# Performance work log

Hardware: AMD Instinct MI355X
Metric: run time of the kernel (lower is better)

## Reference

```python
import jax, jax.numpy as jnp
import numpy as np

N_ATOMS = 500_000
N_DOMAINS = 250_000
N_ENTRIES = 4_000_000
C_IN = 64
C_OUT = 128


def setup_inputs() -> dict:
    key = jax.random.key(0)
    k1, k2, k3, k4 = jax.random.split(key, 4)
    features = jax.random.normal(k1, (N_ATOMS, C_IN), dtype=jnp.float32)
    atom_indices = jax.random.randint(k2, (N_ENTRIES,), 0, N_ATOMS, dtype=jnp.int64)
    domain_ids = jnp.sort(jax.random.randint(k3, (N_ENTRIES,), 0, N_DOMAINS, dtype=jnp.int64))
    # Linear params: xavier_uniform for w, zeros for b (per Linear.reset_parameters)
    limit = jnp.sqrt(6.0 / (C_IN + C_OUT)).astype(jnp.float32)
    W = jax.random.uniform(k4, (C_IN, C_OUT), dtype=jnp.float32, minval=-limit, maxval=limit)
    b = jnp.zeros((C_OUT,), dtype=jnp.float32)
    return {
        "features": features,
        "atom_indices": atom_indices,
        "domain_ids": domain_ids,
        "num_domains": N_DOMAINS,
        "W": W,
        "b": b,
    }


def reference(features, atom_indices, domain_ids, num_domains, W, b):
    # transfer0 (sum reduction): each target domain sums the ptensor0 features
    # of the source atoms it contains. Irregular gather + segment-reduce.
    gathered = features[atom_indices]                       # [E, C_in]
    transferred = jax.ops.segment_sum(gathered, domain_ids,
                                      num_segments=num_domains)  # [M, C_in]
    # Linear projection (mult_factor(0,0)=1 so in_channels unchanged)
    return transferred @ W + b                              # [M, C_out]
```

## Files before the change

kernel.cpp:

```cpp
#include <hip/hip_runtime.h>

__global__ void bounds_kernel(const int* __restrict__ dids,
                              int* __restrict__ starts,
                              int* __restrict__ ends, int E) {
    int e = blockIdx.x * blockDim.x + threadIdx.x;
    if (e >= E) return;
    int d = dids[e];
    if (e == 0) {
        starts[d] = 0;
    } else {
        int dp = dids[e - 1];
        if (d != dp) {
            starts[d] = e;
            ends[dp]  = e;
        }
    }
    if (e == E - 1) ends[d] = E;
}

__global__ void seg_sum_kernel(const float* __restrict__ feat,
                               const int* __restrict__ aidx,
                               const int* __restrict__ starts,
                               const int* __restrict__ ends,
                               float* __restrict__ T, int M) {
    int wid  = (int)(((size_t)blockIdx.x * blockDim.x + threadIdx.x) >> 6);
    if (wid >= M) return;
    int lane = threadIdx.x & 63;
    int g    = lane >> 4;
    int l16  = lane & 15;
    int coff = l16 * 4;

    int s = starts[wid];
    int e = ends[wid];

    float4 acc = make_float4(0.f, 0.f, 0.f, 0.f);
    if (s >= 0) {
        int last = e - 1;
        for (int base = s; base < e; base += 16) {
            int rem = e - base;
            int ti  = base + l16;
            int idxv = aidx[ti <= last ? ti : last];
            if (rem >= 16) {
#pragma unroll
                for (int p = 0; p < 4; ++p) {
                    int row = __shfl(idxv, p * 4 + g, 64);
                    const float4 v =
                        *(const float4*)(feat + (size_t)row * 64 + coff);
                    acc.x += v.x; acc.y += v.y; acc.z += v.z; acc.w += v.w;
                }
            } else {
                int nph = (rem + 3) >> 2;
                for (int p = 0; p < nph; ++p) {
                    int t   = base + p * 4 + g;
                    int row = __shfl(idxv, p * 4 + g, 64);
                    const float4 v =
                        *(const float4*)(feat + (size_t)row * 64 + coff);
                    float w = (t <= last) ? 1.f : 0.f;
                    acc.x = fmaf(v.x, w, acc.x);
                    acc.y = fmaf(v.y, w, acc.y);
                    acc.z = fmaf(v.z, w, acc.z);
                    acc.w = fmaf(v.w, w, acc.w);
                }
            }
        }
        acc.x += __shfl_xor(acc.x, 16, 64);
        acc.y += __shfl_xor(acc.y, 16, 64);
        acc.z += __shfl_xor(acc.z, 16, 64);
        acc.w += __shfl_xor(acc.w, 16, 64);
        acc.x += __shfl_xor(acc.x, 32, 64);
        acc.y += __shfl_xor(acc.y, 32, 64);
        acc.z += __shfl_xor(acc.z, 32, 64);
        acc.w += __shfl_xor(acc.w, 32, 64);
    }
    if (g == 0)
        *(float4*)(T + (size_t)wid * 64 + coff) = acc;
}

#define TM 128
__global__ void __launch_bounds__(256)
proj_kernel(const float* __restrict__ T,
            const float* __restrict__ W,
            const float* __restrict__ bias,
            float* __restrict__ out, int M) {
    __shared__ float lds_w[64][128];
    __shared__ float lds_t[64][TM + 4];

    int tid  = threadIdx.x;
    long row0 = (long)blockIdx.x * TM;

#pragma unroll
    for (int i = 0; i < 8; ++i) {
        int idx = tid + i * 256;
        int k   = idx >> 5;
        int ch  = idx & 31;
        float4 wv = ((const float4*)W)[idx];
        *(float4*)&lds_w[k][ch * 4] = wv;
    }
#pragma unroll
    for (int i = 0; i < 8; ++i) {
        int idx = tid + i * 256;
        int r   = idx >> 4;
        int ch  = idx & 15;
        long gr = row0 + r;
        if (gr > (long)M - 1) gr = (long)M - 1;
        float4 tv = ((const float4*)(T + gr * 64))[ch];
        lds_t[ch * 4 + 0][r] = tv.x;
        lds_t[ch * 4 + 1][r] = tv.y;
        lds_t[ch * 4 + 2][r] = tv.z;
        lds_t[ch * 4 + 3][r] = tv.w;
    }
    __syncthreads();

    int c0 = (tid & 15) * 8;
    int r0 = (tid >> 4) * 8;

    float acc[8][8];
#pragma unroll
    for (int r = 0; r < 8; ++r)
#pragma unroll
        for (int c = 0; c < 8; ++c) acc[r][c] = 0.f;

#pragma unroll 4
    for (int k = 0; k < 64; ++k) {
        float4 ta = *(const float4*)&lds_t[k][r0];
        float4 tb = *(const float4*)&lds_t[k][r0 + 4];
        float4 wa = *(const float4*)&lds_w[k][c0];
        float4 wb = *(const float4*)&lds_w[k][c0 + 4];
        float t[8] = {ta.x, ta.y, ta.z, ta.w, tb.x, tb.y, tb.z, tb.w};
        float w[8] = {wa.x, wa.y, wa.z, wa.w, wb.x, wb.y, wb.z, wb.w};
#pragma unroll
        for (int r = 0; r < 8; ++r)
#pragma unroll
            for (int c = 0; c < 8; ++c)
                acc[r][c] = fmaf(t[r], w[c], acc[r][c]);
    }

    float4 bva = *(const float4*)&bias[c0];
    float4 bvb = *(const float4*)&bias[c0 + 4];
#pragma unroll
    for (int r = 0; r < 8; ++r) {
        long row = row0 + r0 + r;
        if (row < M) {
            float4 o0, o1;
            o0.x = acc[r][0] + bva.x;
            o0.y = acc[r][1] + bva.y;
            o0.z = acc[r][2] + bva.z;
            o0.w = acc[r][3] + bva.w;
            o1.x = acc[r][4] + bvb.x;
            o1.y = acc[r][5] + bvb.y;
            o1.z = acc[r][6] + bvb.z;
            o1.w = acc[r][7] + bvb.w;
            *(float4*)&out[row * 128 + c0]     = o0;
            *(float4*)&out[row * 128 + c0 + 4] = o1;
        }
    }
}

extern "C" void kernel_launch(void* const* d_in, const int* in_sizes, int n_in,
                              void* d_out, int out_size, void* d_ws, size_t ws_size,
                              hipStream_t stream) {
    const float* feat = (const float*)d_in[0];
    const int*   aidx = (const int*)d_in[1];
    const int*   dids = (const int*)d_in[2];
    const float* W    = (const float*)d_in[4];
    const float* bias = (const float*)d_in[5];
    float*       out  = (float*)d_out;

    int E = in_sizes[1];
    int M = out_size / 128;

    float* T = (float*)d_ws;
    size_t tbytes = (size_t)M * 64 * sizeof(float);
    size_t bbytes = 2 * (size_t)M * sizeof(int);

    int* starts;
    if (ws_size >= tbytes + bbytes) {
        starts = (int*)((char*)d_ws + tbytes);
    } else {
        starts = (int*)((char*)d_out + (size_t)out_size * sizeof(float) - bbytes);
    }
    int* ends = starts + M;

    hipMemsetAsync(starts, 0xFF, bbytes, stream);

    bounds_kernel<<<(E + 255) / 256, 256, 0, stream>>>(dids, starts, ends, E);

    int waves_blocks = (int)(((size_t)M * 64 + 255) / 256);
    seg_sum_kernel<<<waves_blocks, 256, 0, stream>>>(feat, aidx, starts, ends, T, M);

    proj_kernel<<<(M + TM - 1) / TM, 256, 0, stream>>>(T, W, bias, out, M);
}
```

Measured before the change: 420.0 us.

## Fuse segment-sum gather with linear projection into a single kernel

Replaces the separate segment-sum and projection kernels with one fused kernel. Each 256-thread block gathers and reduces 128 domains into shared memory, four waves each handling 32 domains in sequence, then runs the 64x128 GEMM tile straight from shared memory. The projection loop is also reorganized to read row-major tiles in float4 chunks of k. This removes the global write and re-read of the intermediate M×64 tensor, but the large shared-memory footprint limits waves per CU during the latency-bound random gather.

After: 580.8 us. +38.3%, slower.

```diff
diff --git a/kernel.cpp b/kernel.cpp
--- a/kernel.cpp
+++ b/kernel.cpp
@@ -18,75 +18,39 @@
     if (e == E - 1) ends[d] = E;
 }
 
-__global__ void seg_sum_kernel(const float* __restrict__ feat,
-                               const int* __restrict__ aidx,
-                               const int* __restrict__ starts,
-                               const int* __restrict__ ends,
-                               float* __restrict__ T, int M) {
-    int wid  = (int)(((size_t)blockIdx.x * blockDim.x + threadIdx.x) >> 6);
-    if (wid >= M) return;
-    int lane = threadIdx.x & 63;
-    int g    = lane >> 4;
-    int l16  = lane & 15;
-    int coff = l16 * 4;
+#define DPB 128
 
-    int s = starts[wid];
-    int e = ends[wid];
+#define KSTEP(J, COMP)                                               \
+    {                                                                \
+        float4 wa = *(const float4*)&lds_w[kq * 4 + J][c0];          \
+        float4 wb = *(const float4*)&lds_w[kq * 4 + J][c0 + 4];      \
+        _Pragma("unroll")                                            \
+        for (int r = 0; r < 8; ++r) {                                \
+            float tv = tr[r].COMP;                                   \
+            acc[r][0] = fmaf(tv, wa.x, acc[r][0]);                   \
+            acc[r][1] = fmaf(tv, wa.y, acc[r][1]);                   \
+            acc[r][2] = fmaf(tv, wa.z, acc[r][2]);                   \
+            acc[r][3] = fmaf(tv, wa.w, acc[r][3]);                   \
+            acc[r][4] = fmaf(tv, wb.x, acc[r][4]);                   \
+            acc[r][5] = fmaf(tv, wb.y, acc[r][5]);                   \
+            acc[r][6] = fmaf(tv, wb.z, acc[r][6]);                   \
+            acc[r][7] = fmaf(tv, wb.w, acc[r][7]);                   \
+        }                                                            \
+    }
 
-    float4 acc = make_float4(0.f, 0.f, 0.f, 0.f);
-    if (s >= 0) {
-        int last = e - 1;
-        for (int base = s; base < e; base += 16) {
-            int rem = e - base;
-            int ti  = base + l16;
-            int idxv = aidx[ti <= last ? ti : last];
-            if (rem >= 16) {
-#pragma unroll
-                for (int p = 0; p < 4; ++p) {
-                    int row = __shfl(idxv, p * 4 + g, 64);
-                    const float4 v =
-                        *(const float4*)(feat + (size_t)row * 64 + coff);
-                    acc.x += v.x; acc.y += v.y; acc.z += v.z; acc.w += v.w;
-                }
-            } else {
-                int nph = (rem + 3) >> 2;
-                for (int p = 0; p < nph; ++p) {
-                    int t   = base + p * 4 + g;
-                    int row = __shfl(idxv, p * 4 + g, 64);
-                    const float4 v =
-                        *(const float4*)(feat + (size_t)row * 64 + coff);
-                    float w = (t <= last) ? 1.f : 0.f;
-                    acc.x = fmaf(v.x, w, acc.x);
-                    acc.y = fmaf(v.y, w, acc.y);
-                    acc.z = fmaf(v.z, w, acc.z);
-                    acc.w = fmaf(v.w, w, acc.w);
-                }
-            }
-        }
-        acc.x += __shfl_xor(acc.x, 16, 64);
-        acc.y += __shfl_xor(acc.y, 16, 64);
-        acc.z += __shfl_xor(acc.z, 16, 64);
-        acc.w += __shfl_xor(acc.w, 16, 64);
-        acc.x += __shfl_xor(acc.x, 32, 64);
-        acc.y += __shfl_xor(acc.y, 32, 64);
-        acc.z += __shfl_xor(acc.z, 32, 64);
-        acc.w += __shfl_xor(acc.w, 32, 64);
-    }
-    if (g == 0)
-        *(float4*)(T + (size_t)wid * 64 + coff) = acc;
-}
-
-#define TM 128
 __global__ void __launch_bounds__(256)
-proj_kernel(const float* __restrict__ T,
-            const float* __restrict__ W,
-            const float* __restrict__ bias,
-            float* __restrict__ out, int M) {
+fused_kernel(const float* __restrict__ feat,
+             const int* __restrict__ aidx,
+             const int* __restrict__ starts,
+             const int* __restrict__ ends,
+             const float* __restrict__ W,
+             const float* __restrict__ bias,
+             float* __restrict__ out, int M) {
     __shared__ float lds_w[64][128];
-    __shared__ float lds_t[64][TM + 4];
+    __shared__ float lds_t[DPB][68];
 
     int tid  = threadIdx.x;
-    long row0 = (long)blockIdx.x * TM;
+    long row0 = (long)blockIdx.x * DPB;
 
 #pragma unroll
     for (int i = 0; i < 8; ++i) {
@@ -96,18 +60,61 @@
         float4 wv = ((const float4*)W)[idx];
         *(float4*)&lds_w[k][ch * 4] = wv;
     }
+
+    int wv_  = tid >> 6;
+    int lane = tid & 63;
+    int g    = lane >> 4;
+    int l16  = lane & 15;
+    int coff = l16 * 4;
+
+    for (int i = 0; i < 32; ++i) {
+        int  r = wv_ * 32 + i;
+        long d = row0 + r;
+        float4 ga = make_float4(0.f, 0.f, 0.f, 0.f);
+        if (d < M) {
+            int s = starts[d];
+            int e = ends[d];
+            if (s >= 0) {
+                int last = e - 1;
+                for (int base = s; base < e; base += 16) {
+                    int rem = e - base;
+                    int ti  = base + l16;
+                    int idxv = aidx[ti <= last ? ti : last];
+                    if (rem >= 16) {
 #pragma unroll
-    for (int i = 0; i < 8; ++i) {
-        int idx = tid + i * 256;
-        int r   = idx >> 4;
-        int ch  = idx & 15;
-        long gr = row0 + r;
-        if (gr > (long)M - 1) gr = (long)M - 1;
-        float4 tv = ((const float4*)(T + gr * 64))[ch];
-        lds_t[ch * 4 + 0][r] = tv.x;
-        lds_t[ch * 4 + 1][r] = tv.y;
-        lds_t[ch * 4 + 2][r] = tv.z;
-        lds_t[ch * 4 + 3][r] = tv.w;
+                        for (int p = 0; p < 4; ++p) {
+                            int row = __shfl(idxv, p * 4 + g, 64);
+                            const float4 v =
+                                *(const float4*)(feat + (size_t)row * 64 + coff);
+                            ga.x += v.x; ga.y += v.y; ga.z += v.z; ga.w += v.w;
+                        }
+                    } else {
+                        int nph = (rem + 3) >> 2;
+                        for (int p = 0; p < nph; ++p) {
+                            int t   = base + p * 4 + g;
+                            int row = __shfl(idxv, p * 4 + g, 64);
+                            const float4 v =
+                                *(const float4*)(feat + (size_t)row * 64 + coff);
+                            float w = (t <= last) ? 1.f : 0.f;
+                            ga.x = fmaf(v.x, w, ga.x);
+                            ga.y = fmaf(v.y, w, ga.y);
+                            ga.z = fmaf(v.z, w, ga.z);
+                            ga.w = fmaf(v.w, w, ga.w);
+                        }
+                    }
+                }
+                ga.x += __shfl_xor(ga.x, 16, 64);
+                ga.y += __shfl_xor(ga.y, 16, 64);
+                ga.z += __shfl_xor(ga.z, 16, 64);
+                ga.w += __shfl_xor(ga.w, 16, 64);
+                ga.x += __shfl_xor(ga.x, 32, 64);
+                ga.y += __shfl_xor(ga.y, 32, 64);
+                ga.z += __shfl_xor(ga.z, 32, 64);
+                ga.w += __shfl_xor(ga.w, 32, 64);
+            }
+        }
+        if (g == 0)
+            *(float4*)&lds_t[r][coff] = ga;
     }
     __syncthreads();
 
@@ -120,19 +127,16 @@
 #pragma unroll
         for (int c = 0; c < 8; ++c) acc[r][c] = 0.f;
 
-#pragma unroll 4
-    for (int k = 0; k < 64; ++k) {
-        float4 ta = *(const float4*)&lds_t[k][r0];
-        float4 tb = *(const float4*)&lds_t[k][r0 + 4];
-        float4 wa = *(const float4*)&lds_w[k][c0];
-        float4 wb = *(const float4*)&lds_w[k][c0 + 4];
-        float t[8] = {ta.x, ta.y, ta.z, ta.w, tb.x, tb.y, tb.z, tb.w};
-        float w[8] = {wa.x, wa.y, wa.z, wa.w, wb.x, wb.y, wb.z, wb.w};
+#pragma unroll 2
+    for (int kq = 0; kq < 16; ++kq) {
+        float4 tr[8];
 #pragma unroll
         for (int r = 0; r < 8; ++r)
-#pragma unroll
-            for (int c = 0; c < 8; ++c)
-                acc[r][c] = fmaf(t[r], w[c], acc[r][c]);
+            tr[r] = *(const float4*)&lds_t[r0 + r][kq * 4];
+        KSTEP(0, x)
+        KSTEP(1, y)
+        KSTEP(2, z)
+        KSTEP(3, w)
     }
 
     float4 bva = *(const float4*)&bias[c0];
@@ -169,24 +173,15 @@
     int E = in_sizes[1];
     int M = out_size / 128;
 
-    float* T = (float*)d_ws;
-    size_t tbytes = (size_t)M * 64 * sizeof(float);
     size_t bbytes = 2 * (size_t)M * sizeof(int);
-
-    int* starts;
-    if (ws_size >= tbytes + bbytes) {
-        starts = (int*)((char*)d_ws + tbytes);
-    } else {
-        starts = (int*)((char*)d_out + (size_t)out_size * sizeof(float) - bbytes);
-    }
-    int* ends = starts + M;
+    int* starts = (int*)d_ws;
+    int* ends   = starts + M;
 
     hipMemsetAsync(starts, 0xFF, bbytes, stream);
 
     bounds_kernel<<<(E + 255) / 256, 256, 0, stream>>>(dids, starts, ends, E);
 
-    int waves_blocks = (int)(((size_t)M * 64 + 255) / 256);
-    seg_sum_kernel<<<waves_blocks, 256, 0, stream>>>(feat, aidx, starts, ends, T, M);
-
-    proj_kernel<<<(M + TM - 1) / TM, 256, 0, stream>>>(T, W, bias, out, M);
+    int nblocks = (M + DPB - 1) / DPB;
+    fused_kernel<<<nblocks, 256, 0, stream>>>(feat, aidx, starts, ends,
+                                              W, bias, out, M);
 }
```
